# Optimization experiments

Hardware: AMD Instinct MI355X
Metric: run time of the kernel (lower is better)

Reference implementation:

```python
import jax, jax.numpy as jnp
import numpy as np

T, B, F = 128, 128, 1024
ALPHA_BASE, LAMBDA_BASE = 0.97, 0.95
THETA_BASE, BETA_THETA = 0.1, 0.01
RHO, GATE_ALPHA = 0.25, 5.0        # gate_cfg rho_B/rho_C, alpha
NUDGE, PHASE_SCALE = 0.1, 0.02     # gate_cfg additive_nudge, ei_cfg phase_corr_scale
MIX_AMP, MIX_NOV, MIX_INST = 1.0, 0.5, 0.5


def _adaptive_percentile_threshold(score, rho, alpha):
    # keep top-rho fraction per row: tau = (1-rho)-quantile, soft sigmoid gate
    tau = jnp.quantile(score, 1.0 - rho, axis=-1, keepdims=True)
    return jax.nn.sigmoid(alpha * (score - tau)), tau


def setup_inputs() -> dict:
    key = jax.random.key(0)
    k0, k1, k2, k3 = jax.random.split(key, 4)
    return {
        "in_re": jax.random.normal(k0, (T, B, F), jnp.float32),
        "in_im": jax.random.normal(k1, (T, B, F), jnp.float32),
        "r_re": 0.05 * jax.random.normal(k2, (F,), jnp.float32),
        "r_im": 0.05 * jax.random.normal(k3, (F,), jnp.float32),
        "alpha_map": jnp.zeros((F,), jnp.float32),
        "lambda_map": jnp.zeros((F,), jnp.float32),
    }


def reference(in_re, in_im, r_re, r_im, alpha_map, lambda_map):
    sg = jax.lax.stop_gradient
    alpha = jnp.clip(ALPHA_BASE + 0.05 * jnp.tanh(alpha_map), 0.9, 0.995)  # [F]
    lam = jnp.clip(LAMBDA_BASE + 0.05 * jnp.tanh(lambda_map), 0.9, 0.995)  # [F]
    r_conj = jnp.conj(r_re + 1j * r_im)                                    # [F] c64
    theta_base = jnp.full((F,), THETA_BASE, jnp.float32)
    in_field = (in_re + 1j * in_im).astype(jnp.complex64)                  # [T,B,F]

    carry0 = dict(
        X=jnp.zeros((B, F), jnp.complex64),
        sA=jnp.zeros((B, F), jnp.float32),
        sB=jnp.zeros((B, F), jnp.float32),
        sC=jnp.zeros((B, F), jnp.float32),
        theta=theta_base,
        mu=jnp.zeros((F,), jnp.float32),
        var=jnp.full((F,), 0.01, jnp.float32),
        ema_unit=jnp.zeros((F,), jnp.complex64),
        b_usage=jnp.zeros((F,), jnp.float32),
        c_usage=jnp.zeros((F,), jnp.float32),
    )

    def step(c, u):
        X_mid = alpha * c["X"] + u                       # [B,F] c64
        amp = jnp.abs(X_mid)
        unit = jnp.exp(1j * jnp.angle(X_mid))            # unit phase
        # EMA stats (torch.no_grad -> stop_gradient)
        mu = sg(0.9 * c["mu"] + 0.1 * amp.mean(0))
        var = sg(0.9 * c["var"] + 0.1 * ((amp - mu[None]) ** 2).mean(0))
        ema_unit = sg(0.9 * c["ema_unit"] + 0.1 * unit.mean(0))
        plv = jnp.abs(ema_unit)                          # [F]
        zscore = (amp - mu[None]) / (jnp.sqrt(var)[None] + 1e-3)
        instab = (1.0 - plv)[None]
        score = MIX_AMP * amp + MIX_NOV * jnp.abs(zscore) + MIX_INST * instab
        gB, _ = _adaptive_percentile_threshold(score, RHO, GATE_ALPHA)
        gC, _ = _adaptive_percentile_threshold(-score, RHO, GATE_ALPHA)
        XB = X_mid * gB
        XC = X_mid * gC
        sA = lam * c["sA"] + jnp.real(X_mid * r_conj)
        sB = lam * c["sB"] + jnp.real(XB * r_conj)
        sC = lam * c["sC"] + jnp.real(XC * r_conj)
        evA = (sA >= c["theta"]).astype(jnp.float32)
        evB = (sB >= c["theta"]).astype(jnp.float32)
        evC = (sC >= c["theta"]).astype(jnp.float32)
        # threshold homeostasis (no_grad)
        theta = c["theta"] + 0.01 * evB.mean(0) - 0.01 * evC.mean(0)
        theta = jnp.clip(theta - BETA_THETA * (theta - theta_base), 0.01, 10.0)
        # reentry_mode='full': phase correction + additive nudge
        corr = (evB.mean(0) > 0).astype(jnp.float32)[None]  # [1,F]
        XA = X_mid * jnp.exp(1j * PHASE_SCALE * corr)
        XA = XA + NUDGE * (XB * corr)
        b_usage = 0.99 * c["b_usage"] + 0.01 * evB.mean(0)
        c_usage = 0.99 * c["c_usage"] + 0.01 * evC.mean(0)
        new = dict(X=XA, sA=sA, sB=sB, sC=sC, theta=theta, mu=mu, var=var,
                   ema_unit=ema_unit, b_usage=b_usage, c_usage=c_usage)
        return new, sA

    _, sA_seq = jax.lax.scan(step, carry0, in_field)
    return sA_seq  # [T,B,F]
```

## Files before the change

### kernel.cpp

```cpp
#include <hip/hip_runtime.h>
#include <math.h>


#define T_STEPS 128
#define B_DIM   128
#define F_DIM   1024
#define NWG     128
#define NTH     256
#define BF      (B_DIM * F_DIM)

typedef unsigned long long ull;

__device__ __forceinline__ ull ld64(const ull* p) {
  return __hip_atomic_load(p, __ATOMIC_RELAXED, __HIP_MEMORY_SCOPE_AGENT);
}
__device__ __forceinline__ void st64(ull* p, ull v) {
  __hip_atomic_store(p, v, __ATOMIC_RELAXED, __HIP_MEMORY_SCOPE_AGENT);
}

extern "C" __global__ void __launch_bounds__(NTH)
ResonatorABC_82094004896068_kernel(
    const float* __restrict__ in_re, const float* __restrict__ in_im,
    const float* __restrict__ r_re_p, const float* __restrict__ r_im_p,
    const float* __restrict__ alpha_map, const float* __restrict__ lambda_map,
    float* __restrict__ out, ull* __restrict__ ws)
{
  const int tid  = threadIdx.x;
  const int wg   = blockIdx.x;
  const int fl   = tid & 7;
  const int rg   = tid >> 3;
  const int f    = (wg << 3) + fl;
  const int wid  = tid >> 6;
  const int lane = tid & 63;

  ull* score64 = ws;
  ull* tauB64  = ws + BF;
  ull* tauC64  = ws + BF + 128;

  __shared__ __align__(16) float pamp[4][8][4];
  __shared__ __align__(16) float pfin[8][4];
  __shared__ __align__(16) float pev[4][8][2];
  __shared__ __align__(16) float evfin[8][2];
  __shared__ __align__(16) unsigned h[1024];
  __shared__ unsigned wsum[4];
  __shared__ unsigned mmw[4][2];
  __shared__ unsigned tbin[4], tbase[4], tcnt[4];
  __shared__ unsigned lcnt[4];
  __shared__ unsigned lists[4][256];
  __shared__ unsigned resv[4], resf[4];
  __shared__ unsigned rmm[2];
  __shared__ unsigned t2[3];
  __shared__ float tauLds[256];

  const float af = fminf(fmaxf(0.97f + 0.05f * tanhf(alpha_map[f]), 0.90f), 0.995f);
  const float lf = fminf(fmaxf(0.95f + 0.05f * tanhf(lambda_map[f]), 0.90f), 0.995f);
  const float rr = r_re_p[f];
  const float ri = r_im_p[f];
  const float c002 = cosf(0.02f);
  const float s002 = sinf(0.02f);

  float X_re[4] = {0.f,0.f,0.f,0.f}, X_im[4] = {0.f,0.f,0.f,0.f};
  float sA[4] = {0.f,0.f,0.f,0.f}, sB[4] = {0.f,0.f,0.f,0.f}, sC[4] = {0.f,0.f,0.f,0.f};
  float mu = 0.f, var = 0.01f, theta = 0.1f, ema_re = 0.f, ema_im = 0.f;

  int idx[4];
  float ur[4], ui[4];
  #pragma unroll
  for (int k = 0; k < 4; ++k) {
    idx[k] = (rg + 32 * k) * F_DIM + f;
    ur[k] = in_re[idx[k]];
    ui[k] = in_im[idx[k]];
  }

  const unsigned KR[4] = {255u, 256u, 767u, 768u};

  for (int t = 0; t < T_STEPS; ++t) {
    const ull want = (ull)(t + 1);

    *(uint4*)&h[4 * tid] = make_uint4(0u, 0u, 0u, 0u);

    float Xm_re[4], Xm_im[4], proj[4], amp[4], score[4];
    float a0 = 0.f, a1 = 0.f, a2 = 0.f, a3 = 0.f;
    #pragma unroll
    for (int k = 0; k < 4; ++k) {
      Xm_re[k] = af * X_re[k] + ur[k];
      Xm_im[k] = af * X_im[k] + ui[k];
      float amp2 = Xm_re[k] * Xm_re[k] + Xm_im[k] * Xm_im[k];
      amp[k] = sqrtf(amp2);
      float invamp = (amp[k] > 0.f) ? (1.0f / amp[k]) : 0.f;
      float un_re = (amp[k] > 0.f) ? (Xm_re[k] * invamp) : 1.0f;
      float un_im = Xm_im[k] * invamp;
      proj[k] = Xm_re[k] * rr + Xm_im[k] * ri;
      sA[k] = lf * sA[k] + proj[k];
      out[t * BF + idx[k]] = sA[k];
      a0 += amp[k]; a1 += amp2; a2 += un_re; a3 += un_im;
    }
    #pragma unroll
    for (int m = 8; m < 64; m <<= 1) {
      a0 += __shfl_xor(a0, m);
      a1 += __shfl_xor(a1, m);
      a2 += __shfl_xor(a2, m);
      a3 += __shfl_xor(a3, m);
    }
    if (lane < 8) { *(float4*)&pamp[wid][lane][0] = make_float4(a0, a1, a2, a3); }
    __syncthreads();
    if (tid < 32) {
      int sfl = tid >> 2, q = tid & 3;
      pfin[sfl][q] = pamp[0][sfl][q] + pamp[1][sfl][q] + pamp[2][sfl][q] + pamp[3][sfl][q];
    }
    __syncthreads();
    float4 SS = *(const float4*)&pfin[fl][0];
    float m1 = SS.x * 0.0078125f;
    float m2 = SS.y * 0.0078125f;
    mu = 0.9f * mu + 0.1f * m1;
    float vm = m2 - 2.f * mu * m1 + mu * mu;
    vm = fmaxf(vm, 0.f);
    var = 0.9f * var + 0.1f * vm;
    ema_re = 0.9f * ema_re + 0.1f * (SS.z * 0.0078125f);
    ema_im = 0.9f * ema_im + 0.1f * (SS.w * 0.0078125f);
    float plv = sqrtf(ema_re * ema_re + ema_im * ema_im);
    float sden = sqrtf(var) + 1e-3f;
    #pragma unroll
    for (int k = 0; k < 4; ++k) {
      float zs = (amp[k] - mu) / sden;
      score[k] = amp[k] + 0.5f * fabsf(zs) + 0.5f * (1.0f - plv);
      st64(&score64[idx[k]], (want << 32) | (ull)__float_as_uint(score[k]));
    }

    float ur_n[4] = {0.f,0.f,0.f,0.f}, ui_n[4] = {0.f,0.f,0.f,0.f};
    if (t + 1 < T_STEPS) {
      #pragma unroll
      for (int k = 0; k < 4; ++k) {
        ur_n[k] = in_re[(t + 1) * BF + idx[k]];
        ui_n[k] = in_im[(t + 1) * BF + idx[k]];
      }
    }

    unsigned uval[4], bin[4];
    {
      const ull* sp0 = &score64[wg * F_DIM + tid];
      #pragma unroll
      for (int k = 0; k < 4; ++k) {
        ull v = ld64(sp0 + 256 * k);
        while ((v >> 32) != want) { __builtin_amdgcn_s_sleep(1); v = ld64(sp0 + 256 * k); }
        uval[k] = (unsigned)v;
      }
    }
    unsigned umin = min(min(uval[0], uval[1]), min(uval[2], uval[3]));
    unsigned umax = max(max(uval[0], uval[1]), max(uval[2], uval[3]));
    #pragma unroll
    for (int m = 1; m < 64; m <<= 1) {
      umin = min(umin, (unsigned)__shfl_xor((int)umin, m));
      umax = max(umax, (unsigned)__shfl_xor((int)umax, m));
    }
    if (lane == 0) { mmw[wid][0] = umin; mmw[wid][1] = umax; }
    __syncthreads();
    unsigned lo = min(min(mmw[0][0], mmw[1][0]), min(mmw[2][0], mmw[3][0]));
    unsigned hi = max(max(mmw[0][1], mmw[1][1]), max(mmw[2][1], mmw[3][1]));

    if (lo != hi) {
      ull rng = (ull)hi - (ull)lo + 1ull;
      ull inv = (1ull << 40) / rng;
      #pragma unroll
      for (int k = 0; k < 4; ++k) {
        bin[k] = (unsigned)((((ull)(uval[k] - lo)) * inv) >> 30);
        atomicAdd(&h[bin[k]], 1u);
      }
      if (tid < 4) { lcnt[tid] = 0u; resf[tid] = 0u; }
      __syncthreads();
      uint4 hc = *(const uint4*)&h[4 * tid];
      unsigned s4 = hc.x + hc.y + hc.z + hc.w;
      unsigned incl = s4;
      #pragma unroll
      for (int d = 1; d < 64; d <<= 1) {
        unsigned vv = __shfl_up(incl, d);
        if (lane >= d) incl += vv;
      }
      if (lane == 63) wsum[wid] = incl;
      __syncthreads();
      unsigned woff = 0u;
      for (int w = 0; w < 4; ++w) if (w < wid) woff += wsum[w];
      unsigned gexcl = woff + incl - s4;
      unsigned cv[4] = {hc.x, hc.y, hc.z, hc.w};
      unsigned bb[4];
      bb[0] = gexcl; bb[1] = bb[0] + cv[0]; bb[2] = bb[1] + cv[1]; bb[3] = bb[2] + cv[2];
      #pragma unroll
      for (int i = 0; i < 4; ++i) {
        if (cv[i] > 0u) {
          #pragma unroll
          for (int r = 0; r < 4; ++r) {
            if (bb[i] <= KR[r] && KR[r] < bb[i] + cv[i]) {
              tbin[r] = 4 * tid + i; tbase[r] = bb[i]; tcnt[r] = cv[i];
            }
          }
        }
      }
      __syncthreads();
      unsigned b0 = tbin[0], b1 = tbin[1], b2 = tbin[2], b3 = tbin[3];
      #pragma unroll
      for (int k = 0; k < 4; ++k) {
        unsigned bk = bin[k], uv = uval[k];
        if (bk == b0) { unsigned s = atomicAdd(&lcnt[0], 1u); if (s < 256u) lists[0][s] = uv; }
        else if (bk == b1 && b1 != b0) { unsigned s = atomicAdd(&lcnt[1], 1u); if (s < 256u) lists[1][s] = uv; }
        else if (bk == b2 && b2 != b1) { unsigned s = atomicAdd(&lcnt[2], 1u); if (s < 256u) lists[2][s] = uv; }
        else if (bk == b3 && b3 != b2) { unsigned s = atomicAdd(&lcnt[3], 1u); if (s < 256u) lists[3][s] = uv; }
      }
      __syncthreads();
      {
        const int j = wid;
        int src = j;
        while (src > 0 && tbin[src - 1] == tbin[j]) --src;
        unsigned c = tcnt[j];
        if (c <= 256u) {
          unsigned kk = KR[j] - tbase[j];
          for (int bi = 0; bi < (int)c; bi += 64) {
            int i = bi + lane;
            if (i < (int)c) {
              unsigned e = lists[src][i];
              unsigned r = 0;
              for (int q = 0; q < (int)c; ++q) {
                unsigned x = lists[src][q];
                r += (x < e || (x == e && q < i)) ? 1u : 0u;
              }
              if (r == kk) { resv[j] = e; resf[j] = 1u; }
            }
          }
        }
      }
      __syncthreads();
      for (int j = 0; j < 4; ++j) {
        if (resf[j]) continue;
        bool inj[4];
        #pragma unroll
        for (int k = 0; k < 4; ++k) inj[k] = (bin[k] == tbin[j]);
        unsigned krem = KR[j] - tbase[j];
        for (int iter = 0; iter < 40; ++iter) {
          if (tid == 0) { rmm[0] = 0xFFFFFFFFu; rmm[1] = 0u; }
          __syncthreads();
          #pragma unroll
          for (int k = 0; k < 4; ++k)
            if (inj[k]) { atomicMin(&rmm[0], uval[k]); atomicMax(&rmm[1], uval[k]); }
          __syncthreads();
          unsigned wlo = rmm[0], whi = rmm[1];
          if (wlo == whi) { if (tid == 0) { resv[j] = wlo; resf[j] = 1u; } __syncthreads(); break; }
          *(uint4*)&h[4 * tid] = make_uint4(0u, 0u, 0u, 0u);
          __syncthreads();
          ull rng2 = (ull)whi - (ull)wlo + 1ull;
          ull inv2 = (1ull << 40) / rng2;
          unsigned nb[4];
          #pragma unroll
          for (int k = 0; k < 4; ++k) {
            nb[k] = inj[k] ? (unsigned)((((ull)(uval[k] - wlo)) * inv2) >> 30) : 0u;
            if (inj[k]) atomicAdd(&h[nb[k]], 1u);
          }
          __syncthreads();
          uint4 hc2 = *(const uint4*)&h[4 * tid];
          unsigned s42 = hc2.x + hc2.y + hc2.z + hc2.w;
          unsigned incl2 = s42;
          #pragma unroll
          for (int d = 1; d < 64; d <<= 1) {
            unsigned vv = __shfl_up(incl2, d);
            if (lane >= d) incl2 += vv;
          }
          if (lane == 63) wsum[wid] = incl2;
          if (tid == 0) lcnt[0] = 0u;
          __syncthreads();
          unsigned woff2 = 0u;
          for (int w = 0; w < 4; ++w) if (w < wid) woff2 += wsum[w];
          unsigned gexcl2 = woff2 + incl2 - s42;
          unsigned cv2[4] = {hc2.x, hc2.y, hc2.z, hc2.w};
          unsigned bb2[4];
          bb2[0] = gexcl2; bb2[1] = bb2[0] + cv2[0]; bb2[2] = bb2[1] + cv2[1]; bb2[3] = bb2[2] + cv2[2];
          #pragma unroll
          for (int i = 0; i < 4; ++i) {
            if (cv2[i] > 0u && bb2[i] <= krem && krem < bb2[i] + cv2[i]) {
              t2[0] = 4 * tid + i; t2[1] = bb2[i]; t2[2] = cv2[i];
            }
          }
          __syncthreads();
          unsigned nbin = t2[0], nbase = t2[1], ncnt = t2[2];
          bool newin[4];
          #pragma unroll
          for (int k = 0; k < 4; ++k) newin[k] = inj[k] && (nb[k] == nbin);
          if (ncnt <= 256u) {
            #pragma unroll
            for (int k = 0; k < 4; ++k)
              if (newin[k]) { unsigned s = atomicAdd(&lcnt[0], 1u); if (s < 256u) lists[0][s] = uval[k]; }
            __syncthreads();
            if (wid == 0) {
              unsigned kk2 = krem - nbase;
              for (int bi = 0; bi < (int)ncnt; bi += 64) {
                int i = bi + lane;
                if (i < (int)ncnt) {
                  unsigned e = lists[0][i];
                  unsigned r = 0;
                  for (int q = 0; q < (int)ncnt; ++q) {
                    unsigned x = lists[0][q];
                    r += (x < e || (x == e && q < i)) ? 1u : 0u;
                  }
                  if (r == kk2) { resv[j] = e; resf[j] = 1u; }
                }
              }
            }
            __syncthreads();
            break;
          }
          #pragma unroll
          for (int k = 0; k < 4; ++k) inj[k] = newin[k];
          krem -= nbase;
        }
      }
    } else {
      if (tid < 4) { resv[tid] = lo; resf[tid] = 1u; }
      __syncthreads();
    }
    if (tid == 0) {
      float s255 = __uint_as_float(resv[0]);
      float s256 = __uint_as_float(resv[1]);
      float s767 = __uint_as_float(resv[2]);
      float s768 = __uint_as_float(resv[3]);
      float tb = 0.75f * s767 + 0.25f * s768;
      float tc = -(0.75f * s256 + 0.25f * s255);
      st64(&tauB64[wg], (want << 32) | (ull)__float_as_uint(tb));
      st64(&tauC64[wg], (want << 32) | (ull)__float_as_uint(tc));
    }

    {
      const ull* src = (tid < 128) ? &tauB64[tid] : &tauC64[tid - 128];
      ull v2 = ld64(src);
      while ((v2 >> 32) != want) { __builtin_amdgcn_s_sleep(1); v2 = ld64(src); }
      tauLds[tid] = __uint_as_float((unsigned)v2);
    }
    __syncthreads();

    float gB[4];
    float e0 = 0.f, e1 = 0.f;
    #pragma unroll
    for (int k = 0; k < 4; ++k) {
      float tb = tauLds[rg + 32 * k];
      float tc = tauLds[128 + rg + 32 * k];
      float sc = score[k];
      gB[k] = 1.0f / (1.0f + expf(-5.0f * (sc - tb)));
      float gC = 1.0f / (1.0f + expf(-5.0f * (-sc - tc)));
      sB[k] = lf * sB[k] + proj[k] * gB[k];
      sC[k] = lf * sC[k] + proj[k] * gC;
      e0 += (sB[k] >= theta) ? 1.0f : 0.0f;
      e1 += (sC[k] >= theta) ? 1.0f : 0.0f;
    }
    #pragma unroll
    for (int m = 8; m < 64; m <<= 1) {
      e0 += __shfl_xor(e0, m);
      e1 += __shfl_xor(e1, m);
    }
    if (lane < 8) { pev[wid][lane][0] = e0; pev[wid][lane][1] = e1; }
    __syncthreads();
    if (tid < 16) {
      int sfl = tid >> 1, q = tid & 1;
      evfin[sfl][q] = pev[0][sfl][q] + pev[1][sfl][q] + pev[2][sfl][q] + pev[3][sfl][q];
    }
    __syncthreads();
    float cB = evfin[fl][0];
    float cC = evfin[fl][1];
    float th1 = theta + 0.01f * (cB * 0.0078125f) - 0.01f * (cC * 0.0078125f);
    theta = fminf(fmaxf(th1 - 0.01f * (th1 - 0.1f), 0.01f), 10.0f);
    bool corr = (cB > 0.f);
    #pragma unroll
    for (int k = 0; k < 4; ++k) {
      float fac_re = corr ? (c002 + 0.1f * gB[k]) : 1.0f;
      float fac_im = corr ? s002 : 0.0f;
      X_re[k] = Xm_re[k] * fac_re - Xm_im[k] * fac_im;
      X_im[k] = Xm_re[k] * fac_im + Xm_im[k] * fac_re;
      ur[k] = ur_n[k]; ui[k] = ui_n[k];
    }
  }
}

extern "C" void kernel_launch(void* const* d_in, const int* in_sizes, int n_in,
                              void* d_out, int out_size, void* d_ws, size_t ws_size,
                              hipStream_t stream) {
  const float* in_re = (const float*)d_in[0];
  const float* in_im = (const float*)d_in[1];
  const float* r_re  = (const float*)d_in[2];
  const float* r_im  = (const float*)d_in[3];
  const float* amap  = (const float*)d_in[4];
  const float* lmap  = (const float*)d_in[5];
  float* out = (float*)d_out;
  ull* ws = (ull*)d_ws;
  hipMemsetAsync(d_ws, 0, (size_t)(BF + 256) * 8, stream);
  hipLaunchKernelGGL(ResonatorABC_82094004896068_kernel,
                     dim3(NWG), dim3(NTH), 0, stream,
                     in_re, in_im, r_re, r_im, amap, lmap, out, ws);
}
```

Before: 1.208 ms.

## Halve workgroup count with 512 threads, selecting two score rows per block

```diff
diff --git a/kernel.cpp b/kernel.cpp
--- a/kernel.cpp
+++ b/kernel.cpp
@@ -5,8 +5,8 @@
 #define T_STEPS 128
 #define B_DIM   128
 #define F_DIM   1024
-#define NWG     128
-#define NTH     256
+#define NWG     64
+#define NTH     512
 #define BF      (B_DIM * F_DIM)
 
 typedef unsigned long long ull;
@@ -27,29 +27,31 @@
 {
   const int tid  = threadIdx.x;
   const int wg   = blockIdx.x;
-  const int fl   = tid & 7;
-  const int rg   = tid >> 3;
-  const int f    = (wg << 3) + fl;
+  const int fl   = tid & 15;
+  const int rg   = tid >> 4;
+  const int f    = (wg << 4) + fl;
   const int wid  = tid >> 6;
   const int lane = tid & 63;
+  const int half = tid >> 8;
+  const int t2   = tid & 255;
+  const int wid2 = t2 >> 6;
 
   ull* score64 = ws;
   ull* tauB64  = ws + BF;
   ull* tauC64  = ws + BF + 128;
 
-  __shared__ __align__(16) float pamp[4][8][4];
-  __shared__ __align__(16) float pfin[8][4];
-  __shared__ __align__(16) float pev[4][8][2];
-  __shared__ __align__(16) float evfin[8][2];
-  __shared__ __align__(16) unsigned h[1024];
-  __shared__ unsigned wsum[4];
-  __shared__ unsigned mmw[4][2];
-  __shared__ unsigned tbin[4], tbase[4], tcnt[4];
-  __shared__ unsigned lcnt[4];
-  __shared__ unsigned lists[4][256];
-  __shared__ unsigned resv[4], resf[4];
-  __shared__ unsigned rmm[2];
-  __shared__ unsigned t2[3];
+  __shared__ __align__(16) float pamp[8][16][4];
+  __shared__ __align__(16) float pfin[16][4];
+  __shared__ __align__(16) float pev[8][16][2];
+  __shared__ __align__(16) float evfin[16][2];
+  __shared__ __align__(16) unsigned h2[2][1024];
+  __shared__ unsigned wsum2[2][4];
+  __shared__ unsigned mmh[2][4][2];
+  __shared__ unsigned tbin2[2][4], tbase2[2][4], tcnt2[2][4];
+  __shared__ unsigned lcnt2[2][4];
+  __shared__ unsigned lists2[2][4][256];
+  __shared__ unsigned resv2[2][4], resf2[2][4];
+  __shared__ unsigned wred[8];
   __shared__ float tauLds[256];
 
   const float af = fminf(fmaxf(0.97f + 0.05f * tanhf(alpha_map[f]), 0.90f), 0.995f);
@@ -73,11 +75,12 @@
   }
 
   const unsigned KR[4] = {255u, 256u, 767u, 768u};
+  const int srow = 2 * wg + half;
 
   for (int t = 0; t < T_STEPS; ++t) {
     const ull want = (ull)(t + 1);
 
-    *(uint4*)&h[4 * tid] = make_uint4(0u, 0u, 0u, 0u);
+    *(uint4*)&(((unsigned*)h2)[4 * tid]) = make_uint4(0u, 0u, 0u, 0u);
 
     float Xm_re[4], Xm_im[4], proj[4], amp[4], score[4];
     float a0 = 0.f, a1 = 0.f, a2 = 0.f, a3 = 0.f;
@@ -96,17 +99,20 @@
       a0 += amp[k]; a1 += amp2; a2 += un_re; a3 += un_im;
     }
     #pragma unroll
-    for (int m = 8; m < 64; m <<= 1) {
+    for (int m = 16; m < 64; m <<= 1) {
       a0 += __shfl_xor(a0, m);
       a1 += __shfl_xor(a1, m);
       a2 += __shfl_xor(a2, m);
       a3 += __shfl_xor(a3, m);
     }
-    if (lane < 8) { *(float4*)&pamp[wid][lane][0] = make_float4(a0, a1, a2, a3); }
-    __syncthreads();
-    if (tid < 32) {
+    if (lane < 16) { *(float4*)&pamp[wid][lane][0] = make_float4(a0, a1, a2, a3); }
+    __syncthreads();
+    if (tid < 64) {
       int sfl = tid >> 2, q = tid & 3;
-      pfin[sfl][q] = pamp[0][sfl][q] + pamp[1][sfl][q] + pamp[2][sfl][q] + pamp[3][sfl][q];
+      float s = 0.f;
+      #pragma unroll
+      for (int w = 0; w < 8; ++w) s += pamp[w][sfl][q];
+      pfin[sfl][q] = s;
     }
     __syncthreads();
     float4 SS = *(const float4*)&pfin[fl][0];
@@ -138,12 +144,17 @@
 
     unsigned uval[4], bin[4];
     {
-      const ull* sp0 = &score64[wg * F_DIM + tid];
-      #pragma unroll
-      for (int k = 0; k < 4; ++k) {
-        ull v = ld64(sp0 + 256 * k);
-        while ((v >> 32) != want) { __builtin_amdgcn_s_sleep(1); v = ld64(sp0 + 256 * k); }
-        uval[k] = (unsigned)v;
+      const ull* sp0 = &score64[srow * F_DIM + t2];
+      ull v[4]; bool ok[4] = {false, false, false, false};
+      int remaining = 4;
+      while (remaining) {
+        #pragma unroll
+        for (int k = 0; k < 4; ++k) if (!ok[k]) v[k] = ld64(sp0 + 256 * k);
+        #pragma unroll
+        for (int k = 0; k < 4; ++k) {
+          if (!ok[k] && (v[k] >> 32) == want) { ok[k] = true; uval[k] = (unsigned)v[k]; --remaining; }
+        }
+        if (remaining) __builtin_amdgcn_s_sleep(1);
       }
     }
     unsigned umin = min(min(uval[0], uval[1]), min(uval[2], uval[3]));
@@ -153,179 +164,128 @@
       umin = min(umin, (unsigned)__shfl_xor((int)umin, m));
       umax = max(umax, (unsigned)__shfl_xor((int)umax, m));
     }
-    if (lane == 0) { mmw[wid][0] = umin; mmw[wid][1] = umax; }
-    __syncthreads();
-    unsigned lo = min(min(mmw[0][0], mmw[1][0]), min(mmw[2][0], mmw[3][0]));
-    unsigned hi = max(max(mmw[0][1], mmw[1][1]), max(mmw[2][1], mmw[3][1]));
-
-    if (lo != hi) {
-      ull rng = (ull)hi - (ull)lo + 1ull;
-      ull inv = (1ull << 40) / rng;
-      #pragma unroll
-      for (int k = 0; k < 4; ++k) {
-        bin[k] = (unsigned)((((ull)(uval[k] - lo)) * inv) >> 30);
-        atomicAdd(&h[bin[k]], 1u);
-      }
-      if (tid < 4) { lcnt[tid] = 0u; resf[tid] = 0u; }
-      __syncthreads();
-      uint4 hc = *(const uint4*)&h[4 * tid];
-      unsigned s4 = hc.x + hc.y + hc.z + hc.w;
-      unsigned incl = s4;
-      #pragma unroll
-      for (int d = 1; d < 64; d <<= 1) {
-        unsigned vv = __shfl_up(incl, d);
-        if (lane >= d) incl += vv;
-      }
-      if (lane == 63) wsum[wid] = incl;
-      __syncthreads();
-      unsigned woff = 0u;
-      for (int w = 0; w < 4; ++w) if (w < wid) woff += wsum[w];
-      unsigned gexcl = woff + incl - s4;
-      unsigned cv[4] = {hc.x, hc.y, hc.z, hc.w};
-      unsigned bb[4];
-      bb[0] = gexcl; bb[1] = bb[0] + cv[0]; bb[2] = bb[1] + cv[1]; bb[3] = bb[2] + cv[2];
-      #pragma unroll
-      for (int i = 0; i < 4; ++i) {
-        if (cv[i] > 0u) {
-          #pragma unroll
-          for (int r = 0; r < 4; ++r) {
-            if (bb[i] <= KR[r] && KR[r] < bb[i] + cv[i]) {
-              tbin[r] = 4 * tid + i; tbase[r] = bb[i]; tcnt[r] = cv[i];
-            }
+    if (lane == 0) { mmh[half][wid2][0] = umin; mmh[half][wid2][1] = umax; }
+    if (tid < 8) { lcnt2[tid >> 2][tid & 3] = 0u; resf2[tid >> 2][tid & 3] = 0u; }
+    __syncthreads();
+    unsigned lo = min(min(mmh[half][0][0], mmh[half][1][0]), min(mmh[half][2][0], mmh[half][3][0]));
+    unsigned hi = max(max(mmh[half][0][1], mmh[half][1][1]), max(mmh[half][2][1], mmh[half][3][1]));
+
+    ull rng = (ull)hi - (ull)lo + 1ull;
+    ull inv = (rng > 1ull) ? ((1ull << 40) / rng) : (1ull << 40);
+    #pragma unroll
+    for (int k = 0; k < 4; ++k) {
+      bin[k] = (unsigned)((((ull)(uval[k] - lo)) * inv) >> 30);
+      atomicAdd(&h2[half][bin[k]], 1u);
+    }
+    __syncthreads();
+    uint4 hc = *(const uint4*)&h2[half][4 * t2];
+    unsigned s4 = hc.x + hc.y + hc.z + hc.w;
+    unsigned incl = s4;
+    #pragma unroll
+    for (int d = 1; d < 64; d <<= 1) {
+      unsigned vv = __shfl_up(incl, d);
+      if (lane >= d) incl += vv;
+    }
+    if (lane == 63) wsum2[half][wid2] = incl;
+    __syncthreads();
+    unsigned woff = 0u;
+    for (int w = 0; w < 4; ++w) if (w < wid2) woff += wsum2[half][w];
+    unsigned gexcl = woff + incl - s4;
+    unsigned cv[4] = {hc.x, hc.y, hc.z, hc.w};
+    unsigned bb[4];
+    bb[0] = gexcl; bb[1] = bb[0] + cv[0]; bb[2] = bb[1] + cv[1]; bb[3] = bb[2] + cv[2];
+    #pragma unroll
+    for (int i = 0; i < 4; ++i) {
+      if (cv[i] > 0u) {
+        #pragma unroll
+        for (int r = 0; r < 4; ++r) {
+          if (bb[i] <= KR[r] && KR[r] < bb[i] + cv[i]) {
+            tbin2[half][r] = 4 * t2 + i; tbase2[half][r] = bb[i]; tcnt2[half][r] = cv[i];
           }
         }
       }
-      __syncthreads();
-      unsigned b0 = tbin[0], b1 = tbin[1], b2 = tbin[2], b3 = tbin[3];
+    }
+    __syncthreads();
+    {
+      unsigned b0 = tbin2[half][0], b1 = tbin2[half][1], b2 = tbin2[half][2], b3 = tbin2[half][3];
       #pragma unroll
       for (int k = 0; k < 4; ++k) {
         unsigned bk = bin[k], uv = uval[k];
-        if (bk == b0) { unsigned s = atomicAdd(&lcnt[0], 1u); if (s < 256u) lists[0][s] = uv; }
-        else if (bk == b1 && b1 != b0) { unsigned s = atomicAdd(&lcnt[1], 1u); if (s < 256u) lists[1][s] = uv; }
-        else if (bk == b2 && b2 != b1) { unsigned s = atomicAdd(&lcnt[2], 1u); if (s < 256u) lists[2][s] = uv; }
-        else if (bk == b3 && b3 != b2) { unsigned s = atomicAdd(&lcnt[3], 1u); if (s < 256u) lists[3][s] = uv; }
-      }
-      __syncthreads();
-      {
-        const int j = wid;
-        int src = j;
-        while (src > 0 && tbin[src - 1] == tbin[j]) --src;
-        unsigned c = tcnt[j];
-        if (c <= 256u) {
-          unsigned kk = KR[j] - tbase[j];
-          for (int bi = 0; bi < (int)c; bi += 64) {
-            int i = bi + lane;
-            if (i < (int)c) {
-              unsigned e = lists[src][i];
-              unsigned r = 0;
-              for (int q = 0; q < (int)c; ++q) {
-                unsigned x = lists[src][q];
-                r += (x < e || (x == e && q < i)) ? 1u : 0u;
-              }
-              if (r == kk) { resv[j] = e; resf[j] = 1u; }
+        if (bk == b0) { unsigned s = atomicAdd(&lcnt2[half][0], 1u); if (s < 256u) lists2[half][0][s] = uv; }
+        else if (bk == b1 && b1 != b0) { unsigned s = atomicAdd(&lcnt2[half][1], 1u); if (s < 256u) lists2[half][1][s] = uv; }
+        else if (bk == b2 && b2 != b1) { unsigned s = atomicAdd(&lcnt2[half][2], 1u); if (s < 256u) lists2[half][2][s] = uv; }
+        else if (bk == b3 && b3 != b2) { unsigned s = atomicAdd(&lcnt2[half][3], 1u); if (s < 256u) lists2[half][3][s] = uv; }
+      }
+    }
+    __syncthreads();
+    {
+      const int hh = half, j = wid2;
+      int src = j;
+      while (src > 0 && tbin2[hh][src - 1] == tbin2[hh][j]) --src;
+      unsigned c = tcnt2[hh][j];
+      if (c <= 256u) {
+        unsigned kk = KR[j] - tbase2[hh][j];
+        for (int bi = 0; bi < (int)c; bi += 64) {
+          int i = bi + lane;
+          if (i < (int)c) {
+            unsigned e = lists2[hh][src][i];
+            unsigned r = 0;
+            for (int q = 0; q < (int)c; ++q) {
+              unsigned x = lists2[hh][src][q];
+              r += (x < e || (x == e && q < i)) ? 1u : 0u;
             }
+            if (r == kk) { resv2[hh][j] = e; resf2[hh][j] = 1u; }
           }
         }
       }
-      __syncthreads();
+    }
+    __syncthreads();
+
+    for (int hh = 0; hh < 2; ++hh) {
       for (int j = 0; j < 4; ++j) {
-        if (resf[j]) continue;
-        bool inj[4];
+        if (resf2[hh][j]) continue;
+        bool cand[4];
         #pragma unroll
-        for (int k = 0; k < 4; ++k) inj[k] = (bin[k] == tbin[j]);
-        unsigned krem = KR[j] - tbase[j];
-        for (int iter = 0; iter < 40; ++iter) {
-          if (tid == 0) { rmm[0] = 0xFFFFFFFFu; rmm[1] = 0u; }
-          __syncthreads();
+        for (int k = 0; k < 4; ++k) cand[k] = (half == hh) && (bin[k] == tbin2[hh][j]);
+        unsigned krem = KR[j] - tbase2[hh][j];
+        unsigned val = 0u;
+        for (int bit = 30; bit >= 0; --bit) {
+          unsigned c0 = 0u;
           #pragma unroll
           for (int k = 0; k < 4; ++k)
-            if (inj[k]) { atomicMin(&rmm[0], uval[k]); atomicMax(&rmm[1], uval[k]); }
+            if (cand[k] && (((uval[k] >> bit) & 1u) == 0u)) ++c0;
+          #pragma unroll
+          for (int d = 1; d < 64; d <<= 1) c0 += (unsigned)__shfl_xor((int)c0, d);
+          if (lane == 0) wred[wid] = c0;
           __syncthreads();
-          unsigned wlo = rmm[0], whi = rmm[1];
-          if (wlo == whi) { if (tid == 0) { resv[j] = wlo; resf[j] = 1u; } __syncthreads(); break; }
-          *(uint4*)&h[4 * tid] = make_uint4(0u, 0u, 0u, 0u);
+          unsigned cnt0 = 0u;
+          #pragma unroll
+          for (int w = 0; w < 8; ++w) cnt0 += wred[w];
+          unsigned chosen = (krem < cnt0) ? 0u : 1u;
+          if (chosen) krem -= cnt0; else val = val;
+          val |= (chosen << bit);
+          #pragma unroll
+          for (int k = 0; k < 4; ++k)
+            cand[k] = cand[k] && (((uval[k] >> bit) & 1u) == chosen);
           __syncthreads();
-          ull rng2 = (ull)whi - (ull)wlo + 1ull;
-          ull inv2 = (1ull << 40) / rng2;
-          unsigned nb[4];
-          #pragma unroll
-          for (int k = 0; k < 4; ++k) {
-            nb[k] = inj[k] ? (unsigned)((((ull)(uval[k] - wlo)) * inv2) >> 30) : 0u;
-            if (inj[k]) atomicAdd(&h[nb[k]], 1u);
-          }
-          __syncthreads();
-          uint4 hc2 = *(const uint4*)&h[4 * tid];
-          unsigned s42 = hc2.x + hc2.y + hc2.z + hc2.w;
-          unsigned incl2 = s42;
-          #pragma unroll
-          for (int d = 1; d < 64; d <<= 1) {
-            unsigned vv = __shfl_up(incl2, d);
-            if (lane >= d) incl2 += vv;
-          }
-          if (lane == 63) wsum[wid] = incl2;
-          if (tid == 0) lcnt[0] = 0u;
-          __syncthreads();
-          unsigned woff2 = 0u;
-          for (int w = 0; w < 4; ++w) if (w < wid) woff2 += wsum[w];
-          unsigned gexcl2 = woff2 + incl2 - s42;
-          unsigned cv2[4] = {hc2.x, hc2.y, hc2.z, hc2.w};
-          unsigned bb2[4];
-          bb2[0] = gexcl2; bb2[1] = bb2[0] + cv2[0]; bb2[2] = bb2[1] + cv2[1]; bb2[3] = bb2[2] + cv2[2];
-          #pragma unroll
-          for (int i = 0; i < 4; ++i) {
-            if (cv2[i] > 0u && bb2[i] <= krem && krem < bb2[i] + cv2[i]) {
-              t2[0] = 4 * tid + i; t2[1] = bb2[i]; t2[2] = cv2[i];
-            }
-          }
-          __syncthreads();
-          unsigned nbin = t2[0], nbase = t2[1], ncnt = t2[2];
-          bool newin[4];
-          #pragma unroll
-          for (int k = 0; k < 4; ++k) newin[k] = inj[k] && (nb[k] == nbin);
-          if (ncnt <= 256u) {
-            #pragma unroll
-            for (int k = 0; k < 4; ++k)
-              if (newin[k]) { unsigned s = atomicAdd(&lcnt[0], 1u); if (s < 256u) lists[0][s] = uval[k]; }
-            __syncthreads();
-            if (wid == 0) {
-              unsigned kk2 = krem - nbase;
-              for (int bi = 0; bi < (int)ncnt; bi += 64) {
-                int i = bi + lane;
-                if (i < (int)ncnt) {
-                  unsigned e = lists[0][i];
-                  unsigned r = 0;
-                  for (int q = 0; q < (int)ncnt; ++q) {
-                    unsigned x = lists[0][q];
-                    r += (x < e || (x == e && q < i)) ? 1u : 0u;
-                  }
-                  if (r == kk2) { resv[j] = e; resf[j] = 1u; }
-                }
-              }
-            }
-            __syncthreads();
-            break;
-          }
-          #pragma unroll
-          for (int k = 0; k < 4; ++k) inj[k] = newin[k];
-          krem -= nbase;
         }
-      }
-    } else {
-      if (tid < 4) { resv[tid] = lo; resf[tid] = 1u; }
-      __syncthreads();
-    }
-    if (tid == 0) {
-      float s255 = __uint_as_float(resv[0]);
-      float s256 = __uint_as_float(resv[1]);
-      float s767 = __uint_as_float(resv[2]);
-      float s768 = __uint_as_float(resv[3]);
+        if (tid == 0) { resv2[hh][j] = val; resf2[hh][j] = 1u; }
+        __syncthreads();
+      }
+    }
+
+    if (t2 == 0) {
+      float s255 = __uint_as_float(resv2[half][0]);
+      float s256 = __uint_as_float(resv2[half][1]);
+      float s767 = __uint_as_float(resv2[half][2]);
+      float s768 = __uint_as_float(resv2[half][3]);
       float tb = 0.75f * s767 + 0.25f * s768;
       float tc = -(0.75f * s256 + 0.25f * s255);
-      st64(&tauB64[wg], (want << 32) | (ull)__float_as_uint(tb));
-      st64(&tauC64[wg], (want << 32) | (ull)__float_as_uint(tc));
-    }
-
-    {
+      st64(&tauB64[srow], (want << 32) | (ull)__float_as_uint(tb));
+      st64(&tauC64[srow], (want << 32) | (ull)__float_as_uint(tc));
+    }
+
+    if (tid < 256) {
       const ull* src = (tid < 128) ? &tauB64[tid] : &tauC64[tid - 128];
       ull v2 = ld64(src);
       while ((v2 >> 32) != want) { __builtin_amdgcn_s_sleep(1); v2 = ld64(src); }
@@ -348,15 +308,18 @@
       e1 += (sC[k] >= theta) ? 1.0f : 0.0f;
     }
     #pragma unroll
-    for (int m = 8; m < 64; m <<= 1) {
+    for (int m = 16; m < 64; m <<= 1) {
       e0 += __shfl_xor(e0, m);
       e1 += __shfl_xor(e1, m);
     }
-    if (lane < 8) { pev[wid][lane][0] = e0; pev[wid][lane][1] = e1; }
-    __syncthreads();
-    if (tid < 16) {
+    if (lane < 16) { pev[wid][lane][0] = e0; pev[wid][lane][1] = e1; }
+    __syncthreads();
+    if (tid < 32) {
       int sfl = tid >> 1, q = tid & 1;
-      evfin[sfl][q] = pev[0][sfl][q] + pev[1][sfl][q] + pev[2][sfl][q] + pev[3][sfl][q];
+      float s = 0.f;
+      #pragma unroll
+      for (int w = 0; w < 8; ++w) s += pev[w][sfl][q];
+      evfin[sfl][q] = s;
     }
     __syncthreads();
     float cB = evfin[fl][0];
```

Result: slower. 1.388 ms (+14.9%).
